# Optimization experiments

Measured on AMD Instinct MI355X. Metric: run time of the kernel, lower is better.

The kernel has to match this reference:

```python
import jax, jax.numpy as jnp
import numpy as np
from jax.scipy.special import gammaln, logsumexp

T, K, D = 262144, 32, 64


def setup_inputs() -> dict:
    key = jax.random.key(0)
    ks = jax.random.split(key, 7)
    Y = jax.random.normal(ks[0], (T, D), dtype=jnp.float32)
    dT = jax.random.uniform(ks[1], (T,), dtype=jnp.float32) + 0.01  # strictly positive intervals
    A = jax.random.normal(ks[2], (K, K), dtype=jnp.float32)
    log_ab = jax.random.normal(ks[3], (K, 2), dtype=jnp.float32) * 0.5
    mu = jax.random.normal(ks[4], (K, D), dtype=jnp.float32)
    log_sigma = jax.random.normal(ks[5], (K, D), dtype=jnp.float32) * 0.1
    pi = jax.random.normal(ks[6], (K,), dtype=jnp.float32)
    return {"Y": Y, "dT": dT, "A": A, "log_ab": log_ab, "mu": mu, "log_sigma": log_sigma, "pi": pi}


def _gamma_ll(dT, log_ab):
    # per-state Gamma(concentration=exp(log_ab[:,0]), rate=exp(log_ab[:,1])) log_prob -> [T, K]
    a = jnp.exp(log_ab[:, 0])
    b = jnp.exp(log_ab[:, 1])
    const = a * log_ab[:, 1] - gammaln(a)  # a*log(b) - lgamma(a)
    return const[None, :] + jnp.log(dT)[:, None] * (a - 1.0)[None, :] - dT[:, None] * b[None, :]


def _gauss_ll(Y, mu, log_sigma):
    # diagonal-Gaussian emission log-likelihood summed over D, via GEMMs -> [T, K]
    inv_var = jnp.exp(-2.0 * log_sigma)  # [K, D]
    quad = (-0.5) * (Y * Y) @ inv_var.T + Y @ (mu * inv_var).T - 0.5 * jnp.sum(mu * mu * inv_var, axis=-1)[None, :]
    const = -jnp.sum(log_sigma, axis=-1) - 0.5 * D * jnp.log(2.0 * jnp.pi).astype(Y.dtype)
    return quad + const[None, :]


def _hmm_lognorm(pi0, logA, ll):
    # log-domain forward algorithm; returns log normalizer (scalar)
    alpha0 = pi0 + ll[0]

    def step(alpha, ll_t):
        # alpha_t[j] = logsumexp_i(alpha[i] + logA[i, j]) + ll_t[j]
        alpha = logsumexp(alpha[:, None] + logA, axis=0) + ll_t
        return alpha, None

    alphaT, _ = jax.lax.scan(step, alpha0, ll[1:])
    return logsumexp(alphaT)


def reference(Y, dT, A, log_ab, mu, log_sigma, pi):
    h = Y  # obs_model embedding (identity for Gaussian emission model)
    y_ll = _gauss_ll(Y, mu, log_sigma)          # [T, K]
    y_loss = jnp.zeros((), dtype=Y.dtype)
    dT_ll = _gamma_ll(dT, log_ab)               # [T, K]
    ll = y_ll + dT_ll
    logA = jax.nn.log_softmax(A, axis=1)        # LogSoftmax(dim=1)(A)
    pi0 = jax.nn.log_softmax(pi, axis=0)        # LogSoftmax(dim=0)(pi)
    loss = -1.0 * _hmm_lognorm(pi0, logA, ll) + y_loss
    return h, loss
```

## Files before the change

### kernel.cpp

```cpp
#include <hip/hip_runtime.h>
#include <stdint.h>

#define TT 262144
#define KK 32
#define DD 64
#define LSTEP 32
#define PCH 8192
#define YSTRIDE 68

typedef __attribute__((ext_vector_type(4)))  float f4v;
typedef __attribute__((ext_vector_type(16))) float f16v;
typedef __attribute__((ext_vector_type(4)))  short s4v;
typedef __attribute__((ext_vector_type(2)))  int   i2v;
typedef __attribute__((ext_vector_type(2)))  unsigned int u2v;
typedef __attribute__((ext_vector_type(4)))  unsigned int u4v;

#define WS_AFRAG_US 0
#define WS_WFRAG_US 1024
#define WS_WF    2560
#define WS_CK    6656
#define WS_AM1   6688
#define WS_BB    6720
#define WS_PI0   6752
#define WS_LS    8192
#define WS_LS2   16384
#define SH_MATS  33280
#define SH_MATS2 (33280 + PCH*1024)
#define LN2F 0.69314718055994531f

__device__ __forceinline__ unsigned pkbf(float hi, float lo) {
    return __builtin_amdgcn_perm(__builtin_bit_cast(unsigned, hi),
                                 __builtin_bit_cast(unsigned, lo), 0x07060302u);
}
__device__ __forceinline__ unsigned short f2bf_rne(float f) {
    unsigned u = __builtin_bit_cast(unsigned, f);
    unsigned r = u + 0x7FFFu + ((u >> 16) & 1u);
    return (unsigned short)(r >> 16);
}
__device__ __forceinline__ float bf2f(unsigned short u) {
    return __builtin_bit_cast(float, (unsigned)u << 16);
}
__device__ __forceinline__ float wmax32(float v) {
    v = fmaxf(v, __shfl_xor(v, 1));  v = fmaxf(v, __shfl_xor(v, 2));
    v = fmaxf(v, __shfl_xor(v, 4));  v = fmaxf(v, __shfl_xor(v, 8));
    v = fmaxf(v, __shfl_xor(v, 16));
    return v;
}
__device__ __forceinline__ float wmax64(float v) {
    v = wmax32(v); v = fmaxf(v, __shfl_xor(v, 32));
    return v;
}
__device__ __forceinline__ float wsum32(float v) {
    v += __shfl_xor(v, 1); v += __shfl_xor(v, 2); v += __shfl_xor(v, 4);
    v += __shfl_xor(v, 8); v += __shfl_xor(v, 16);
    return v;
}
__device__ __forceinline__ float wsum64(float v) {
    v = wsum32(v); v += __shfl_xor(v, 32);
    return v;
}
__device__ __forceinline__ float wval(int dd, int k, const float* mu, const float* lsg) {
    int d = dd & 63;
    float lv = lsg[k * DD + d];
    float iv = __expf(-2.f * lv);
    return (dd < DD) ? (-0.5f * iv) : (mu[k * DD + d] * iv);
}

__global__ void k0_prep(const float* __restrict__ Y, const float* __restrict__ A,
                        const float* __restrict__ lab, const float* __restrict__ mu,
                        const float* __restrict__ lsg, const float* __restrict__ pi,
                        float* __restrict__ ws, float* __restrict__ out)
{
    __shared__ float lseA[KK];
    const int tid = threadIdx.x;
    if (tid < KK) {
        float m = -1e30f;
        for (int j = 0; j < KK; ++j) m = fmaxf(m, A[tid * KK + j]);
        float s = 0.f;
        for (int j = 0; j < KK; ++j) s += __expf(A[tid * KK + j] - m);
        lseA[tid] = m + __logf(s);

        float mp = -1e30f;
        for (int j = 0; j < KK; ++j) mp = fmaxf(mp, pi[j]);
        float sp = 0.f;
        for (int j = 0; j < KK; ++j) sp += __expf(pi[j] - mp);
        ws[WS_PI0 + tid] = pi[tid] - (mp + __logf(sp));

        float la = lab[tid * 2 + 0], lb = lab[tid * 2 + 1];
        float a = __expf(la), b = __expf(lb);
        float c1 = 0.f, c2 = 0.f;
        for (int d = 0; d < DD; ++d) {
            float lv = lsg[tid * DD + d];
            float mv = mu[tid * DD + d];
            c1 -= lv;
            c2 += mv * mv * __expf(-2.f * lv);
        }
        ws[WS_CK + tid]  = a * lb - lgammaf(a) + c1 - 0.5f * c2 - 32.f * 1.8378770664093453f;
        ws[WS_AM1 + tid] = a - 1.f;
        ws[WS_BB + tid]  = b;
    }
    __syncthreads();
    unsigned short* us = (unsigned short*)ws;
    for (int idx = tid; idx < 1024; idx += 256) {
        int g = idx >> 8, rem = idx & 255, ln = rem >> 2, e = rem & 3;
        int m = 8 * g + 4 * (ln >> 5) + e, i = ln & 31;
        us[WS_AFRAG_US + idx] = f2bf_rne(__expf(A[m * KK + i] - lseA[m]));
    }
    for (int idx = tid; idx < 4096; idx += 256) {
        int s = idx >> 8, rem = idx & 255, ln = rem >> 2, e = rem & 3;
        int dd = 8 * s + 4 * (ln >> 5) + e, k = ln & 31;
        us[WS_WFRAG_US + idx] = f2bf_rne(wval(dd, k, mu, lsg));
    }
    for (int idx = tid; idx < 4096; idx += 256) {
        int dd = idx >> 5, k = idx & 31;
        ws[WS_WF + idx] = wval(dd, k, mu, lsg);
    }
    if (tid < DD) out[tid] = Y[tid];
}

__global__ __launch_bounds__(256, 4) void k1_scan(
    const float* __restrict__ Y, const float* __restrict__ dTp,
    float* __restrict__ ws, float* __restrict__ out)
{
    __shared__ __align__(16) float Yt[4][32 * YSTRIDE];
    __shared__ __align__(16) float dtv[4][32], dtl[4][32];

    const int tid = threadIdx.x;
    const int wv = tid >> 6, l = tid & 63, h = l >> 5, c = l & 31;
    const int p = blockIdx.x * 4 + wv;
    const int t0 = 1 + p * LSTEP;
    const int nsteps = min(LSTEP, TT - t0);

    const unsigned short* afr = (const unsigned short*)ws + WS_AFRAG_US;
    const unsigned short* wfr = (const unsigned short*)ws + WS_WFRAG_US;

    const float cK = ws[WS_CK + c], am1 = ws[WS_AM1 + c], bb = ws[WS_BB + c];

    if (l < 32) {
        int t = t0 + l;
        float dv = (t < TT) ? dTp[t] : 1.f;
        dtv[wv][l] = dv;
        dtl[wv][l] = __logf(dv);
    }

    f16v zf;
    #pragma unroll
    for (int r = 0; r < 16; ++r) zf[r] = 0.f;

    {
        const size_t gbase = (size_t)t0 * DD;
        const int r = (l >> 4);
        const int col = (l & 15) * 4;
        #pragma unroll
        for (int i = 0; i < 8; ++i) {
            const size_t gi = gbase + (size_t)i * 256 + l * 4;
            f4v y4; y4[0] = 0.f; y4[1] = 0.f; y4[2] = 0.f; y4[3] = 0.f;
            const bool ok = gi < (size_t)TT * DD;
            if (ok) y4 = *(const f4v*)(Y + gi);
            if (ok) *(f4v*)(out + gi) = y4;
            *(f4v*)(&Yt[wv][(i * 4 + r) * YSTRIDE + col]) = y4;
        }
    }

    f16v acc = zf;
    s4v rawf[8];
    #pragma unroll
    for (int g = 0; g < 8; ++g) {
        const f4v y4 = *(const f4v*)(&Yt[wv][c * YSTRIDE + 8 * g + 4 * h]);
        const f4v q4 = y4 * y4;
        i2v sq; sq[0] = pkbf(q4[1], q4[0]); sq[1] = pkbf(q4[3], q4[2]);
        i2v rw; rw[0] = pkbf(y4[1], y4[0]); rw[1] = pkbf(y4[3], y4[2]);
        rawf[g] = __builtin_bit_cast(s4v, rw);
        s4v wf = *(const s4v*)(wfr + g * 256 + l * 4);
        acc = __builtin_amdgcn_mfma_f32_32x32x8bf16_1k(__builtin_bit_cast(s4v, sq), wf, acc, 0, 0, 0);
    }
    #pragma unroll
    for (int g = 0; g < 8; ++g) {
        s4v wf = *(const s4v*)(wfr + (8 + g) * 256 + l * 4);
        acc = __builtin_amdgcn_mfma_f32_32x32x8bf16_1k(rawf[g], wf, acc, 0, 0, 0);
    }

    s4v aF[4];
    #pragma unroll
    for (int g = 0; g < 4; ++g) aF[g] = *(const s4v*)(afr + g * 256 + l * 4);

    float csv = 0.f;
    #pragma unroll
    for (int m = 0; m < 4; ++m) {
        const f4v dv4 = *(const f4v*)(&dtv[wv][8 * m + 4 * h]);
        const f4v dl4 = *(const f4v*)(&dtl[wv][8 * m + 4 * h]);
        #pragma unroll
        for (int j = 0; j < 4; ++j) {
            const int row = 8 * m + 4 * h + j;
            float llv = acc[4 * m + j] + cK + am1 * dl4[j] - bb * dv4[j];
            float cm = wmax32(llv);
            Yt[wv][row * YSTRIDE + c] = __expf(llv - cm);
            csv += (row < nsteps) ? cm : 0.f;
        }
    }
    float cacc = wsum64(csv) * (1.f / 32.f);

    asm volatile("s_waitcnt lgkmcnt(0)" ::: "memory");

    f16v S;
    #pragma unroll
    for (int m = 0; m < 4; ++m)
        #pragma unroll
        for (int j = 0; j < 4; ++j)
            S[4 * m + j] = ((8 * m + 4 * h + j) == c) ? 1.f : 0.f;
    float l2acc = 0.f;

    auto step = [&](int n) {
        f16v Dv = zf;
        #pragma unroll
        for (int g = 0; g < 4; ++g) {
            i2v bd; bd[0] = pkbf(S[4 * g + 1], S[4 * g + 0]);
                    bd[1] = pkbf(S[4 * g + 3], S[4 * g + 2]);
            Dv = __builtin_amdgcn_mfma_f32_32x32x8bf16_1k(aF[g], __builtin_bit_cast(s4v, bd), Dv, 0, 0, 0);
        }
        #pragma unroll
        for (int m = 0; m < 4; ++m) {
            const f4v e4 = *(const f4v*)(&Yt[wv][n * YSTRIDE + 8 * m + 4 * h]);
            #pragma unroll
            for (int j = 0; j < 4; ++j) S[4 * m + j] = Dv[4 * m + j] * e4[j];
        }
    };
    auto rescale = [&]() {
        float mx = S[0];
        #pragma unroll
        for (int r = 1; r < 16; ++r) mx = fmaxf(mx, S[r]);
        mx = wmax64(mx);
        const float inv = __fdividef(1.f, mx);
        #pragma unroll
        for (int r = 0; r < 16; ++r) S[r] *= inv;
        l2acc += __log2f(mx);
    };

    if (p != PCH - 1) {
        #pragma unroll
        for (int n = 0; n < LSTEP; ++n) {
            step(n);
            if ((n & 3) == 3) rescale();
        }
    } else {
        for (int n = 0; n < nsteps; ++n) {
            step(n);
            if ((n & 3) == 3) rescale();
        }
    }

    unsigned short* Tb = (unsigned short*)&Yt[wv][0];
    asm volatile("s_waitcnt lgkmcnt(0)" ::: "memory");
    #pragma unroll
    for (int m = 0; m < 4; ++m)
        #pragma unroll
        for (int j = 0; j < 4; ++j)
            Tb[(8 * m + 4 * h + j) * 36 + c] = f2bf_rne(S[4 * m + j]);
    asm volatile("s_waitcnt lgkmcnt(0)" ::: "memory");
    u2v tg[4];
    #pragma unroll
    for (int g = 0; g < 4; ++g)
        tg[g] = *(const u2v*)(Tb + c * 36 + 8 * g + 4 * h);
    unsigned short* gm = (unsigned short*)ws + SH_MATS + (size_t)p * 1024 + l * 16;
    u4v s0; s0[0] = tg[0][0]; s0[1] = tg[0][1]; s0[2] = tg[1][0]; s0[3] = tg[1][1];
    u4v s1; s1[0] = tg[2][0]; s1[1] = tg[2][1]; s1[2] = tg[3][0]; s1[3] = tg[3][1];
    *(u4v*)(gm) = s0;
    *(u4v*)(gm + 8) = s1;
    if (l == 0) ws[WS_LS + p] = cacc + LN2F * l2acc;
}

__device__ __forceinline__ f16v prodAU(const u4v a0, const u4v a1, const f16v U, const f16v zf) {
    s4v aA[4];
    u2v t;
    t[0] = a0[0]; t[1] = a0[1]; aA[0] = __builtin_bit_cast(s4v, t);
    t[0] = a0[2]; t[1] = a0[3]; aA[1] = __builtin_bit_cast(s4v, t);
    t[0] = a1[0]; t[1] = a1[1]; aA[2] = __builtin_bit_cast(s4v, t);
    t[0] = a1[2]; t[1] = a1[3]; aA[3] = __builtin_bit_cast(s4v, t);
    f16v Dv = zf;
    #pragma unroll
    for (int g = 0; g < 4; ++g) {
        i2v bd; bd[0] = pkbf(U[4 * g + 1], U[4 * g + 0]);
                bd[1] = pkbf(U[4 * g + 3], U[4 * g + 2]);
        Dv = __builtin_amdgcn_mfma_f32_32x32x8bf16_1k(aA[g], __builtin_bit_cast(s4v, bd), Dv, 0, 0, 0);
    }
    return Dv;
}

__global__ __launch_bounds__(128, 1) void k2_combine(float* __restrict__ ws)
{
    __shared__ __align__(16) unsigned short slot[2][1152];
    __shared__ float scl[2], lac[2];
    const int tid = threadIdx.x, wv = tid >> 6, l = tid & 63, h = l >> 5, c = l & 31;
    const int blk = blockIdx.x;
    const int idx0 = blk * 64 + wv * 32;
    const unsigned short* mats = (const unsigned short*)ws + SH_MATS;

    float lsv = (l < 32) ? ws[WS_LS + idx0 + l] : 0.f;
    float lssum = wsum64(lsv);

    f16v zf;
    #pragma unroll
    for (int r = 0; r < 16; ++r) zf[r] = 0.f;
    f16v U;
    #pragma unroll
    for (int m = 0; m < 4; ++m)
        #pragma unroll
        for (int j = 0; j < 4; ++j)
            U[4 * m + j] = ((8 * m + 4 * h + j) == c) ? 1.f : 0.f;
    float l2a = 0.f;

    u4v pf[2][2];
    {
        const u4v* mp0 = (const u4v*)(mats + (size_t)idx0 * 1024) + l * 2;
        const u4v* mp1 = (const u4v*)(mats + (size_t)(idx0 + 1) * 1024) + l * 2;
        pf[0][0] = mp0[0]; pf[0][1] = mp0[1];
        pf[1][0] = mp1[0]; pf[1][1] = mp1[1];
    }
    for (int q = 0; q < 32; ++q) {
        const u4v a0 = pf[q & 1][0], a1 = pf[q & 1][1];
        if (q + 2 < 32) {
            const u4v* mp = (const u4v*)(mats + (size_t)(idx0 + q + 2) * 1024) + l * 2;
            pf[q & 1][0] = mp[0]; pf[q & 1][1] = mp[1];
        }
        f16v Dv = prodAU(a0, a1, U, zf);
        if ((q & 3) == 3) {
            float mx = Dv[0];
            #pragma unroll
            for (int r = 1; r < 16; ++r) mx = fmaxf(mx, Dv[r]);
            mx = wmax64(mx);
            const float inv = __fdividef(1.f, mx);
            #pragma unroll
            for (int r = 0; r < 16; ++r) U[r] = Dv[r] * inv;
            l2a += __log2f(mx);
        } else {
            U = Dv;
        }
    }
    #pragma unroll
    for (int m = 0; m < 4; ++m)
        #pragma unroll
        for (int j = 0; j < 4; ++j)
            slot[wv][(8 * m + 4 * h + j) * 36 + c] = f2bf_rne(U[4 * m + j]);
    if (l == 0) { scl[wv] = lssum; lac[wv] = l2a; }
    __syncthreads();

    if (wv == 0) {
        u4v a0, a1;
        {
            u2v t0 = *(const u2v*)(&slot[1][c * 36 + 0 + 4 * h]);
            u2v t1 = *(const u2v*)(&slot[1][c * 36 + 8 + 4 * h]);
            u2v t2 = *(const u2v*)(&slot[1][c * 36 + 16 + 4 * h]);
            u2v t3 = *(const u2v*)(&slot[1][c * 36 + 24 + 4 * h]);
            a0[0] = t0[0]; a0[1] = t0[1]; a0[2] = t1[0]; a0[3] = t1[1];
            a1[0] = t2[0]; a1[1] = t2[1]; a1[2] = t3[0]; a1[3] = t3[1];
        }
        f16v Dv = prodAU(a0, a1, U, zf);
        float mx = Dv[0];
        #pragma unroll
        for (int r = 1; r < 16; ++r) mx = fmaxf(mx, Dv[r]);
        mx = wmax64(mx);
        const float inv = __fdividef(1.f, mx);
        #pragma unroll
        for (int r = 0; r < 16; ++r) U[r] = Dv[r] * inv;
        const float l2tot = lac[0] + lac[1] + __log2f(mx);
        asm volatile("s_waitcnt lgkmcnt(0)" ::: "memory");
        #pragma unroll
        for (int m = 0; m < 4; ++m)
            #pragma unroll
            for (int j = 0; j < 4; ++j)
                slot[0][(8 * m + 4 * h + j) * 36 + c] = f2bf_rne(U[4 * m + j]);
        asm volatile("s_waitcnt lgkmcnt(0)" ::: "memory");
        u2v tg[4];
        #pragma unroll
        for (int g = 0; g < 4; ++g)
            tg[g] = *(const u2v*)(&slot[0][c * 36 + 8 * g + 4 * h]);
        unsigned short* gm = (unsigned short*)ws + SH_MATS2 + (size_t)blk * 1024 + l * 16;
        u4v s0; s0[0] = tg[0][0]; s0[1] = tg[0][1]; s0[2] = tg[1][0]; s0[3] = tg[1][1];
        u4v s1; s1[0] = tg[2][0]; s1[1] = tg[2][1]; s1[2] = tg[3][0]; s1[3] = tg[3][1];
        *(u4v*)(gm) = s0;
        *(u4v*)(gm + 8) = s1;
        if (l == 0) ws[WS_LS2 + blk] = scl[0] + scl[1] + LN2F * l2tot;
    }
}

__global__ __launch_bounds__(1024, 1) void k3_final(
    const float* __restrict__ Y, const float* __restrict__ dTp,
    float* __restrict__ ws, float* __restrict__ out)
{
    __shared__ __align__(16) unsigned short slot[16][1152];
    __shared__ float sc[16];
    const int tid = threadIdx.x, wv = tid >> 6, l = tid & 63, h = l >> 5, c = l & 31;
    const unsigned short* mats2 = (const unsigned short*)ws + SH_MATS2;

    f16v zf;
    #pragma unroll
    for (int r = 0; r < 16; ++r) zf[r] = 0.f;

    const int idx0 = wv * 8;
    float lsv = (l < 8) ? ws[WS_LS2 + idx0 + l] : 0.f;
    float lssum = wsum64(lsv);
    f16v U;
    #pragma unroll
    for (int m = 0; m < 4; ++m)
        #pragma unroll
        for (int j = 0; j < 4; ++j)
            U[4 * m + j] = ((8 * m + 4 * h + j) == c) ? 1.f : 0.f;
    float l2a = 0.f;
    u4v pf[2][2];
    {
        const u4v* mp0 = (const u4v*)(mats2 + (size_t)idx0 * 1024) + l * 2;
        const u4v* mp1 = (const u4v*)(mats2 + (size_t)(idx0 + 1) * 1024) + l * 2;
        pf[0][0] = mp0[0]; pf[0][1] = mp0[1];
        pf[1][0] = mp1[0]; pf[1][1] = mp1[1];
    }
    for (int q = 0; q < 8; ++q) {
        const u4v a0 = pf[q & 1][0], a1 = pf[q & 1][1];
        if (q + 2 < 8) {
            const u4v* mp = (const u4v*)(mats2 + (size_t)(idx0 + q + 2) * 1024) + l * 2;
            pf[q & 1][0] = mp[0]; pf[q & 1][1] = mp[1];
        }
        f16v Dv = prodAU(a0, a1, U, zf);
        if ((q & 3) == 3) {
            float mx = Dv[0];
            #pragma unroll
            for (int r = 1; r < 16; ++r) mx = fmaxf(mx, Dv[r]);
            mx = wmax64(mx);
            const float inv = __fdividef(1.f, mx);
            #pragma unroll
            for (int r = 0; r < 16; ++r) U[r] = Dv[r] * inv;
            l2a += __log2f(mx);
        } else {
            U = Dv;
        }
    }
    #pragma unroll
    for (int m = 0; m < 4; ++m)
        #pragma unroll
        for (int j = 0; j < 4; ++j)
            slot[wv][(8 * m + 4 * h + j) * 36 + c] = f2bf_rne(U[4 * m + j]);
    if (l == 0) sc[wv] = lssum + LN2F * l2a;
    __syncthreads();

    for (int s = 1; s < 16; s <<= 1) {
        const int cnt = 16 / (2 * s);
        if (wv < cnt) {
            const int i = wv * 2 * s;
            s4v aA[4], bB[4];
            #pragma unroll
            for (int g = 0; g < 4; ++g) {
                u2v t = *(const u2v*)(&slot[i + s][c * 36 + 8 * g + 4 * h]);
                aA[g] = __builtin_bit_cast(s4v, t);
                s4v b;
                #pragma unroll
                for (int j = 0; j < 4; ++j)
                    b[j] = (short)slot[i][(8 * g + 4 * h + j) * 36 + c];
                bB[g] = b;
            }
            f16v Dv = zf;
            #pragma unroll
            for (int g = 0; g < 4; ++g)
                Dv = __builtin_amdgcn_mfma_f32_32x32x8bf16_1k(aA[g], bB[g], Dv, 0, 0, 0);
            float mx = Dv[0];
            #pragma unroll
            for (int r = 1; r < 16; ++r) mx = fmaxf(mx, Dv[r]);
            mx = wmax64(mx);
            const float inv = __fdividef(1.f, mx);
            #pragma unroll
            for (int m = 0; m < 4; ++m)
                #pragma unroll
                for (int j = 0; j < 4; ++j)
                    slot[i][(8 * m + 4 * h + j) * 36 + c] = f2bf_rne(Dv[4 * m + j] * inv);
            if (l == 0) sc[i] = sc[i] + sc[i + s] + __logf(mx);
        }
        __syncthreads();
    }

    if (wv == 0) {
        float acc = 0.f;
        const float* Wf = ws + WS_WF;
        for (int dd = 0; dd < 128; ++dd) {
            const float yv = Y[dd & 63];
            const float f = (dd < 64) ? yv * yv : yv;
            acc = fmaf(f, Wf[dd * 32 + c], acc);
        }
        const float dt0 = dTp[0];
        const float ll0 = acc + ws[WS_CK + c] + ws[WS_AM1 + c] * __logf(dt0) - ws[WS_BB + c] * dt0;
        const float av = ws[WS_PI0 + c] + ll0;
        const float c0 = wmax32(av);
        const float a0 = __expf(av - c0);
        float part = 0.f;
        #pragma unroll
        for (int i = 0; i < 16; ++i) {
            const int ii = 16 * h + i;
            const float m = bf2f(slot[0][c * 36 + ii]);
            const float ai = __shfl(a0, ii);
            part = fmaf(m, ai, part);
        }
        const float srow = part + __shfl_xor(part, 32);
        const float tot = wsum32(srow);
        if (l == 0) out[(size_t)TT * DD] = -(sc[0] + c0 + __logf(tot));
    }
}

extern "C" void kernel_launch(void* const* d_in, const int* in_sizes, int n_in,
                              void* d_out, int out_size, void* d_ws, size_t ws_size,
                              hipStream_t stream)
{
    const float* Y   = (const float*)d_in[0];
    const float* dTp = (const float*)d_in[1];
    const float* A   = (const float*)d_in[2];
    const float* lab = (const float*)d_in[3];
    const float* mu  = (const float*)d_in[4];
    const float* lsg = (const float*)d_in[5];
    const float* pi  = (const float*)d_in[6];
    float* out = (float*)d_out;
    float* ws  = (float*)d_ws;

    hipLaunchKernelGGL(k0_prep, dim3(1), dim3(256), 0, stream, Y, A, lab, mu, lsg, pi, ws, out);
    hipLaunchKernelGGL(k1_scan, dim3(PCH / 4), dim3(256), 0, stream, Y, dTp, ws, out);
    hipLaunchKernelGGL(k2_combine, dim3(128), dim3(128), 0, stream, ws);
    hipLaunchKernelGGL(k3_final, dim3(1), dim3(1024), 0, stream, Y, dTp, ws, out);
}
```

Before: 189.1 us.

## Stage Y tile as bf16 in shared memory to raise k1_scan occupancy

Converts the Y tile to bf16 before writing it to LDS, shrinking the per-wave buffer from 32x68 floats to 1152 floats and reusing it for the exp-emission matrix with a 36 stride. The Y^2 fragment is now rebuilt from the bf16 values by squaring, and the two MFMA loops are interleaved so the rawf register array is no longer needed. Launch bounds are raised from 4 to 8 blocks per CU to allow more resident waves. Squaring an already-rounded bf16 value adds slightly more error, and the higher occupancy target may force register spills.

Result: no change. 192.8 us (+1.9%).

```diff
diff --git a/kernel.cpp b/kernel.cpp
--- a/kernel.cpp
+++ b/kernel.cpp
@@ -6,7 +6,6 @@
 #define DD 64
 #define LSTEP 32
 #define PCH 8192
-#define YSTRIDE 68
 
 typedef __attribute__((ext_vector_type(4)))  float f4v;
 typedef __attribute__((ext_vector_type(16))) float f16v;
@@ -118,11 +117,11 @@
     if (tid < DD) out[tid] = Y[tid];
 }
 
-__global__ __launch_bounds__(256, 4) void k1_scan(
+__global__ __launch_bounds__(256, 8) void k1_scan(
     const float* __restrict__ Y, const float* __restrict__ dTp,
     float* __restrict__ ws, float* __restrict__ out)
 {
-    __shared__ __align__(16) float Yt[4][32 * YSTRIDE];
+    __shared__ __align__(16) float buf[4][1152];
     __shared__ __align__(16) float dtv[4][32], dtl[4][32];
 
     const int tid = threadIdx.x;
@@ -142,6 +141,9 @@
         dtv[wv][l] = dv;
         dtl[wv][l] = __logf(dv);
     }
+
+    unsigned short* ybf = (unsigned short*)&buf[wv][0];
+    float* E = &buf[wv][0];
 
     f16v zf;
     #pragma unroll
@@ -158,31 +160,34 @@
             const bool ok = gi < (size_t)TT * DD;
             if (ok) y4 = *(const f4v*)(Y + gi);
             if (ok) *(f4v*)(out + gi) = y4;
-            *(f4v*)(&Yt[wv][(i * 4 + r) * YSTRIDE + col]) = y4;
-        }
-    }
+            u2v yw; yw[0] = pkbf(y4[1], y4[0]); yw[1] = pkbf(y4[3], y4[2]);
+            const int row = i * 4 + r;
+            *(u2v*)(ybf + row * 72 + col) = yw;
+        }
+    }
+    asm volatile("s_waitcnt lgkmcnt(0)" ::: "memory");
 
     f16v acc = zf;
-    s4v rawf[8];
     #pragma unroll
     for (int g = 0; g < 8; ++g) {
-        const f4v y4 = *(const f4v*)(&Yt[wv][c * YSTRIDE + 8 * g + 4 * h]);
-        const f4v q4 = y4 * y4;
-        i2v sq; sq[0] = pkbf(q4[1], q4[0]); sq[1] = pkbf(q4[3], q4[2]);
-        i2v rw; rw[0] = pkbf(y4[1], y4[0]); rw[1] = pkbf(y4[3], y4[2]);
-        rawf[g] = __builtin_bit_cast(s4v, rw);
-        s4v wf = *(const s4v*)(wfr + g * 256 + l * 4);
-        acc = __builtin_amdgcn_mfma_f32_32x32x8bf16_1k(__builtin_bit_cast(s4v, sq), wf, acc, 0, 0, 0);
-    }
-    #pragma unroll
-    for (int g = 0; g < 8; ++g) {
-        s4v wf = *(const s4v*)(wfr + (8 + g) * 256 + l * 4);
-        acc = __builtin_amdgcn_mfma_f32_32x32x8bf16_1k(rawf[g], wf, acc, 0, 0, 0);
+        const s4v fy = *(const s4v*)(ybf + c * 72 + 8 * g + 4 * h);
+        const s4v wfy = *(const s4v*)(wfr + (8 + g) * 256 + l * 4);
+        acc = __builtin_amdgcn_mfma_f32_32x32x8bf16_1k(fy, wfy, acc, 0, 0, 0);
+        const u2v fu = __builtin_bit_cast(u2v, fy);
+        const float f0 = __builtin_bit_cast(float, fu[0] << 16);
+        const float f1 = __builtin_bit_cast(float, fu[0] & 0xffff0000u);
+        const float f2 = __builtin_bit_cast(float, fu[1] << 16);
+        const float f3 = __builtin_bit_cast(float, fu[1] & 0xffff0000u);
+        u2v qu; qu[0] = pkbf(f1 * f1, f0 * f0); qu[1] = pkbf(f3 * f3, f2 * f2);
+        const s4v wfq = *(const s4v*)(wfr + g * 256 + l * 4);
+        acc = __builtin_amdgcn_mfma_f32_32x32x8bf16_1k(__builtin_bit_cast(s4v, qu), wfq, acc, 0, 0, 0);
     }
 
     s4v aF[4];
     #pragma unroll
     for (int g = 0; g < 4; ++g) aF[g] = *(const s4v*)(afr + g * 256 + l * 4);
+
+    asm volatile("s_waitcnt lgkmcnt(0)" ::: "memory");
 
     float csv = 0.f;
     #pragma unroll
@@ -194,7 +199,7 @@
             const int row = 8 * m + 4 * h + j;
             float llv = acc[4 * m + j] + cK + am1 * dl4[j] - bb * dv4[j];
             float cm = wmax32(llv);
-            Yt[wv][row * YSTRIDE + c] = __expf(llv - cm);
+            E[row * 36 + c] = __expf(llv - cm);
             csv += (row < nsteps) ? cm : 0.f;
         }
     }
@@ -220,7 +225,7 @@
         }
         #pragma unroll
         for (int m = 0; m < 4; ++m) {
-            const f4v e4 = *(const f4v*)(&Yt[wv][n * YSTRIDE + 8 * m + 4 * h]);
+            const f4v e4 = *(const f4v*)(&E[n * 36 + 8 * m + 4 * h]);
             #pragma unroll
             for (int j = 0; j < 4; ++j) S[4 * m + j] = Dv[4 * m + j] * e4[j];
         }
@@ -249,7 +254,7 @@
         }
     }
 
-    unsigned short* Tb = (unsigned short*)&Yt[wv][0];
+    unsigned short* Tb = (unsigned short*)E;
     asm volatile("s_waitcnt lgkmcnt(0)" ::: "memory");
     #pragma unroll
     for (int m = 0; m < 4; ++m)
```
